# Performance work log

Measured on AMD Instinct MI355X. Metric: run time of the kernel, lower is better.

Reference implementation:

```python
import jax, jax.numpy as jnp
import numpy as np

L = 64      # number of physical sites (hilbert.size)
d = 2       # local Hilbert dimension (hilbert.local_size)
D = 8       # bond dimension
CHI = 4     # Kraus dimension
B = 1024    # batch of configurations


def setup_inputs() -> dict:
    key = jax.random.key(0)
    k1, k2 = jax.random.split(key)
    # local quantum-number indices, rows and columns concatenated: [B, 2L]
    qn = jax.random.randint(k1, (B, 2 * L), 0, d, dtype=jnp.int32)
    # MPDO unit-cell tensors: small random perturbation added to identity in the (D, D) slots
    iden = jnp.broadcast_to(jnp.eye(D, dtype=jnp.float32)[None, None, :, :, None], (L, d, D, D, CHI))
    tensors = 0.01 * jax.random.normal(k2, (L, d, D, D, CHI), dtype=jnp.float32) + iden
    return {"qn": qn, "tensors": tensors}


def reference(qn, tensors):
    D2 = D * D
    qn_r = qn[:, :L].T  # [L, B]
    qn_c = qn[:, L:].T  # [L, B]
    edge0 = jnp.broadcast_to(jnp.eye(D2, dtype=tensors.dtype), (qn.shape[0], D2, D2))

    def step(edge, site):
        T, ir, ic = site                 # T: [d, D, D, CHI], ir/ic: [B]
        Tr = T[ir]                       # [B, D, D, CHI]
        Tc = jnp.conj(T[ic])             # [B, D, D, CHI]
        m = jnp.einsum('bijk,blmk->biljm', Tr, Tc).reshape(-1, D2, D2)
        return jnp.matmul(edge, m), None

    step = jax.checkpoint(step)
    edge, _ = jax.lax.scan(step, edge0, (tensors, qn_r, qn_c))
    rho = jnp.trace(edge, axis1=-2, axis2=-1)   # [B]
    return jnp.log(rho.astype(jnp.complex64))
```

## Files before the change

kernel.cpp:

```cpp
#include <hip/hip_runtime.h>
#include <math.h>


#define NSITES 64
#define NPAIRS 32

typedef float f32x16 __attribute__((ext_vector_type(16)));
typedef int   i32x8  __attribute__((ext_vector_type(8)));

union AFrag { uint4 q[2]; i32x8 v; };

#define PACK4(P, A0, A1, A2, A3)                                               \
    asm("v_cvt_pk_fp8_f32 %0, %1, %2" : "=v"(P) : "v"(A0), "v"(A1));           \
    asm("v_cvt_pk_fp8_f32 %0, %1, %2 op_sel:[0,0,1]" : "+v"(P) : "v"(A2), "v"(A3));

#define MFMA64(A, B, C)                                                        \
    __builtin_amdgcn_mfma_scale_f32_32x32x64_f8f6f4(                           \
        (A), (B), (C), 0, 0, 0, 0x7F7F7F7F, 0, 0x7F7F7F7F)

__global__ __launch_bounds__(64)
void mpdo_prep2f8k(const float* __restrict__ T, uint4* __restrict__ Mf8) {
    const int blk = blockIdx.x;
    const int pair = blk >> 4, combo = blk & 15;
    const int c0 = combo >> 2, c1 = combo & 3;
    const int ir0 = c0 >> 1, ic0 = c0 & 1, ir1 = c1 >> 1, ic1 = c1 & 1;
    const int lane = threadIdx.x;
    const int site0 = 2 * pair, site1 = 2 * pair + 1;

    __shared__ float sT0[256], sT1[256], sT2[256], sT3[256];
    __shared__ float sPA[16 * 64], sPB[16 * 64];

    *(float4*)&sT0[lane * 4] = *(const float4*)(T + ((size_t)(site0 * 2 + ir0)) * 256 + lane * 4);
    *(float4*)&sT1[lane * 4] = *(const float4*)(T + ((size_t)(site0 * 2 + ic0)) * 256 + lane * 4);
    *(float4*)&sT2[lane * 4] = *(const float4*)(T + ((size_t)(site1 * 2 + ir1)) * 256 + lane * 4);
    *(float4*)&sT3[lane * 4] = *(const float4*)(T + ((size_t)(site1 * 2 + ic1)) * 256 + lane * 4);
    __syncthreads();

    {
        const int i = lane >> 3, j = lane & 7;
        float pa[4][4], pb[4][4];
#pragma unroll
        for (int k = 0; k < 4; ++k)
#pragma unroll
            for (int jp = 0; jp < 4; ++jp) { pa[k][jp] = 0.0f; pb[k][jp] = 0.0f; }
#pragma unroll
        for (int a = 0; a < 8; ++a) {
            float4 x0 = *(const float4*)&sT0[(i * 8 + a) * 4];
            float4 y0 = *(const float4*)&sT2[(a * 8 + j) * 4];
            float4 x1 = *(const float4*)&sT1[(i * 8 + a) * 4];
            float4 y1 = *(const float4*)&sT3[(a * 8 + j) * 4];
            const float xk0[4] = {x0.x, x0.y, x0.z, x0.w};
            const float yj0[4] = {y0.x, y0.y, y0.z, y0.w};
            const float xk1[4] = {x1.x, x1.y, x1.z, x1.w};
            const float yj1[4] = {y1.x, y1.y, y1.z, y1.w};
#pragma unroll
            for (int k = 0; k < 4; ++k)
#pragma unroll
                for (int jp = 0; jp < 4; ++jp) {
                    pa[k][jp] = fmaf(xk0[k], yj0[jp], pa[k][jp]);
                    pb[k][jp] = fmaf(xk1[k], yj1[jp], pb[k][jp]);
                }
        }
#pragma unroll
        for (int k = 0; k < 4; ++k)
#pragma unroll
            for (int jp = 0; jp < 4; ++jp) {
                sPA[(k * 4 + jp) * 64 + lane] = pa[k][jp];
                sPB[(k * 4 + jp) * 64 + lane] = pb[k][jp];
            }
    }
    __syncthreads();

    const int h = lane >> 5, r = lane & 31, m = r & 7, j2 = r >> 3;
    float acc2[2][32];
#pragma unroll
    for (int ti = 0; ti < 2; ++ti)
#pragma unroll
        for (int e = 0; e < 32; ++e) acc2[ti][e] = 0.0f;

#pragma unroll 4
    for (int c = 0; c < 16; ++c) {
        float pav[2][4], pbv[8];
#pragma unroll
        for (int ti = 0; ti < 2; ++ti)
#pragma unroll
            for (int ii = 0; ii < 4; ++ii)
                pav[ti][ii] = sPA[c * 64 + (4 * h + ii) * 8 + (4 * ti + j2)];
#pragma unroll
        for (int l = 0; l < 8; ++l) pbv[l] = sPB[c * 64 + l * 8 + m];
#pragma unroll
        for (int ti = 0; ti < 2; ++ti)
#pragma unroll
            for (int ii = 0; ii < 4; ++ii)
#pragma unroll
                for (int l = 0; l < 8; ++l)
                    acc2[ti][8 * ii + l] = fmaf(pav[ti][ii], pbv[l], acc2[ti][8 * ii + l]);
    }

#pragma unroll
    for (int ti = 0; ti < 2; ++ti) {
        unsigned dw[8];
#pragma unroll
        for (int j = 0; j < 8; ++j) {
            float v[4];
#pragma unroll
            for (int s = 0; s < 4; ++s) {
                float wv = acc2[ti][4 * j + s] * 0.0625f;
                if (ti == h && (4 * j + s) == r) wv -= 1.0f;
                v[s] = wv;
            }
            PACK4(dw[j], v[0], v[1], v[2], v[3])
        }
        Mf8[((size_t)(pair * 16 + combo) * 4 + ti * 2 + 0) * 64 + lane] =
            make_uint4(dw[0], dw[1], dw[2], dw[3]);
        Mf8[((size_t)(pair * 16 + combo) * 4 + ti * 2 + 1) * 64 + lane] =
            make_uint4(dw[4], dw[5], dw[6], dw[7]);
    }
}

__global__ __launch_bounds__(64, 1)
void mpdo_mfmaK(const int* __restrict__ qn, const uint4* __restrict__ Mf8,
                float* __restrict__ out) {
    const int b = blockIdx.x;
    const int lane = threadIdx.x;
    const int* qb = qn + (size_t)b * (2 * NSITES);
    const int pi = lane & 31;
    const int pc = (qb[2 * pi] << 3) | (qb[64 + 2 * pi] << 2) |
                   (qb[2 * pi + 1] << 1) | (qb[64 + 2 * pi + 1]);
    const unsigned long long m3 = __ballot(pc & 8);
    const unsigned long long m2 = __ballot(pc & 4);
    const unsigned long long m1 = __ballot(pc & 2);
    const unsigned long long m0 = __ballot(pc & 1);
    const int col = lane & 31, hh = lane >> 5;
    const int laneoff = lane * 16;

    f32x16 acc[2][2];
#pragma unroll
    for (int rt = 0; rt < 2; ++rt)
#pragma unroll
        for (int ct = 0; ct < 2; ++ct)
#pragma unroll
            for (int g = 0; g < 16; ++g) {
                int row = (g & 3) + 8 * (g >> 2) + 4 * hh;
                acc[rt][ct][g] = (rt == ct && row == col) ? 1.0f : 0.0f;
            }

    const char* Mbase = (const char*)Mf8;
    AFrag A0[2], A1[2], A2[2];

#define COMBO(T_) ((int)(((((m3) >> (T_)) & 1ull) << 3) | ((((m2) >> (T_)) & 1ull) << 2) | \
                         ((((m1) >> (T_)) & 1ull) << 1) | (((m0) >> (T_)) & 1ull)))
#define LOADF(DST, PIDX)                                                       \
    {                                                                          \
        int c_ = COMBO(PIDX);                                                  \
        const char* nb_ = Mbase + (((size_t)(PIDX) * 16 + c_) << 12) + laneoff;\
        DST[0].q[0] = *(const uint4*)(nb_ + 0 * 1024);                         \
        DST[0].q[1] = *(const uint4*)(nb_ + 1 * 1024);                         \
        DST[1].q[0] = *(const uint4*)(nb_ + 2 * 1024);                         \
        DST[1].q[1] = *(const uint4*)(nb_ + 3 * 1024);                         \
    }

#define MAKE_BCOL(BV, CT)                                                      \
    {                                                                          \
        _Pragma("unroll")                                                      \
        for (int q = 0; q < 4; ++q) {                                          \
            unsigned p0, p1;                                                   \
            PACK4(p0, acc[0][CT][4 * q + 0], acc[0][CT][4 * q + 1],            \
                      acc[0][CT][4 * q + 2], acc[0][CT][4 * q + 3])            \
            PACK4(p1, acc[1][CT][4 * q + 0], acc[1][CT][4 * q + 1],            \
                      acc[1][CT][4 * q + 2], acc[1][CT][4 * q + 3])            \
            asm("v_permlane32_swap_b32 %0, %1" : "+v"(p0), "+v"(p1));          \
            BV[2 * q] = (int)p0; BV[2 * q + 1] = (int)p1;                      \
        }                                                                      \
    }

#define SITE_BODY(T_, CUR, NXT)                                                \
    {                                                                          \
        if ((T_) + 2 < 32) { LOADF(NXT, (T_) + 2) }                            \
        i32x8 b0, b1;                                                          \
        MAKE_BCOL(b0, 0)                                                       \
        MAKE_BCOL(b1, 1)                                                       \
        acc[0][0] = MFMA64(CUR[0].v, b0, acc[0][0]);                           \
        acc[0][1] = MFMA64(CUR[0].v, b1, acc[0][1]);                           \
        acc[1][0] = MFMA64(CUR[1].v, b0, acc[1][0]);                           \
        acc[1][1] = MFMA64(CUR[1].v, b1, acc[1][1]);                           \
    }

    LOADF(A0, 0)
    LOADF(A1, 1)

    SITE_BODY(0,  A0, A2) SITE_BODY(1,  A1, A0) SITE_BODY(2,  A2, A1)
    SITE_BODY(3,  A0, A2) SITE_BODY(4,  A1, A0) SITE_BODY(5,  A2, A1)
    SITE_BODY(6,  A0, A2) SITE_BODY(7,  A1, A0) SITE_BODY(8,  A2, A1)
    SITE_BODY(9,  A0, A2) SITE_BODY(10, A1, A0) SITE_BODY(11, A2, A1)
    SITE_BODY(12, A0, A2) SITE_BODY(13, A1, A0) SITE_BODY(14, A2, A1)
    SITE_BODY(15, A0, A2) SITE_BODY(16, A1, A0) SITE_BODY(17, A2, A1)
    SITE_BODY(18, A0, A2) SITE_BODY(19, A1, A0) SITE_BODY(20, A2, A1)
    SITE_BODY(21, A0, A2) SITE_BODY(22, A1, A0) SITE_BODY(23, A2, A1)
    SITE_BODY(24, A0, A2) SITE_BODY(25, A1, A0) SITE_BODY(26, A2, A1)
    SITE_BODY(27, A0, A2) SITE_BODY(28, A1, A0) SITE_BODY(29, A2, A1)
    SITE_BODY(30, A0, A2) SITE_BODY(31, A1, A0)
#undef SITE_BODY
#undef MAKE_BCOL
#undef LOADF
#undef COMBO

    float diag = 0.0f;
#pragma unroll
    for (int tt = 0; tt < 2; ++tt)
#pragma unroll
        for (int g = 0; g < 16; ++g) {
            int row = (g & 3) + 8 * (g >> 2) + 4 * hh;
            if (row == col) diag += acc[tt][tt][g];
        }
#pragma unroll
    for (int off = 32; off >= 1; off >>= 1)
        diag += __shfl_xor(diag, off, 64);

    if (lane == 0) {
        float tr = diag;
        float re = logf(fabsf(tr)) + 64.0f * 1.3862943611198906f;
        float im = (tr < 0.0f) ? 3.14159265358979323846f : 0.0f;
        out[2 * b]     = re;
        out[2 * b + 1] = im;
    }
}

#define DD 8
#define KCHI 4
__global__ __launch_bounds__(64, 1)
void mpdo_chain(const int* __restrict__ qn, const float* __restrict__ T,
                float* __restrict__ out) {
    const int b = blockIdx.x;
    const int lane = threadIdx.x;
    __shared__ float sA[KCHI][DD][DD];
    __shared__ float sB[KCHI][DD][DD];
    float E[DD][DD];
#pragma unroll
    for (int i = 0; i < DD; ++i)
#pragma unroll
        for (int l = 0; l < DD; ++l) E[i][l] = (i * DD + l == lane) ? 1.0f : 0.0f;
    const int* qb = qn + (size_t)b * (2 * NSITES);
    int ir0 = qb[0], ic0 = qb[NSITES];
    float4 aP = *reinterpret_cast<const float4*>(T + (size_t)ir0 * 256 + lane * 4);
    float4 bP = *reinterpret_cast<const float4*>(T + (size_t)ic0 * 256 + lane * 4);
    const int li = lane >> 3, lj = lane & 7;
#pragma unroll 1
    for (int site = 0; site < NSITES; ++site) {
        __syncthreads();
        sA[0][li][lj] = 0.5f * aP.x; sA[1][li][lj] = 0.5f * aP.y;
        sA[2][li][lj] = 0.5f * aP.z; sA[3][li][lj] = 0.5f * aP.w;
        sB[0][li][lj] = 0.5f * bP.x; sB[1][li][lj] = 0.5f * bP.y;
        sB[2][li][lj] = 0.5f * bP.z; sB[3][li][lj] = 0.5f * bP.w;
        __syncthreads();
        if (site + 1 < NSITES) {
            int irn = qb[site + 1], icn = qb[NSITES + site + 1];
            aP = *reinterpret_cast<const float4*>(T + ((size_t)(site + 1) * 2 + irn) * 256 + lane * 4);
            bP = *reinterpret_cast<const float4*>(T + ((size_t)(site + 1) * 2 + icn) * 256 + lane * 4);
        }
        float Ep[DD][DD];
#pragma unroll
        for (int j = 0; j < DD; ++j)
#pragma unroll
            for (int m = 0; m < DD; ++m) Ep[j][m] = 0.0f;
#pragma unroll 1
        for (int k = 0; k < KCHI; ++k) {
            float tmp[DD][DD];
#pragma unroll
            for (int l = 0; l < DD; ++l) {
                const float4* bp = reinterpret_cast<const float4*>(&sB[k][l][0]);
                float4 b0 = bp[0], b1 = bp[1];
                float brow[DD] = {b0.x, b0.y, b0.z, b0.w, b1.x, b1.y, b1.z, b1.w};
                if (l == 0) {
#pragma unroll
                    for (int i = 0; i < DD; ++i)
#pragma unroll
                        for (int m = 0; m < DD; ++m) tmp[i][m] = E[i][0] * brow[m];
                } else {
#pragma unroll
                    for (int i = 0; i < DD; ++i)
#pragma unroll
                        for (int m = 0; m < DD; ++m)
                            tmp[i][m] = fmaf(E[i][l], brow[m], tmp[i][m]);
                }
            }
#pragma unroll
            for (int i = 0; i < DD; ++i) {
                const float4* ap = reinterpret_cast<const float4*>(&sA[k][i][0]);
                float4 a0 = ap[0], a1 = ap[1];
                float arow[DD] = {a0.x, a0.y, a0.z, a0.w, a1.x, a1.y, a1.z, a1.w};
#pragma unroll
                for (int j = 0; j < DD; ++j)
#pragma unroll
                    for (int m = 0; m < DD; ++m)
                        Ep[j][m] = fmaf(arow[j], tmp[i][m], Ep[j][m]);
            }
        }
#pragma unroll
        for (int i = 0; i < DD; ++i)
#pragma unroll
            for (int l = 0; l < DD; ++l) E[i][l] = Ep[i][l];
    }
    float diag = 0.0f;
#pragma unroll
    for (int i = 0; i < DD; ++i)
#pragma unroll
        for (int l = 0; l < DD; ++l) diag += (i * DD + l == lane) ? E[i][l] : 0.0f;
#pragma unroll
    for (int off = 32; off >= 1; off >>= 1) diag += __shfl_xor(diag, off, 64);
    if (lane == 0) {
        float tr = diag;
        out[2 * b]     = logf(fabsf(tr)) + 64.0f * 1.3862943611198906f;
        out[2 * b + 1] = (tr < 0.0f) ? 3.14159265358979323846f : 0.0f;
    }
}

extern "C" void kernel_launch(void* const* d_in, const int* in_sizes, int n_in,
                              void* d_out, int out_size, void* d_ws, size_t ws_size,
                              hipStream_t stream) {
    const int*   qn  = (const int*)d_in[0];
    const float* T   = (const float*)d_in[1];
    float*       out = (float*)d_out;
    const int B = in_sizes[0] / (2 * NSITES);
    const size_t WS_F8 = (size_t)NPAIRS * 16 * 4 * 64 * 16;
    if (ws_size >= WS_F8) {
        uint4* Mf8 = (uint4*)d_ws;
        mpdo_prep2f8k<<<dim3(NPAIRS * 16), dim3(64), 0, stream>>>(T, Mf8);
        mpdo_mfmaK<<<dim3(B), dim3(64), 0, stream>>>(qn, Mf8, out);
    } else {
        mpdo_chain<<<dim3(B), dim3(64), 0, stream>>>(qn, T, out);
    }
}
```

Before: 26.00 us.

## Split site chain into two independent halves interleaved for MFMA latency hiding

The 32-step serial chain of 64x64 FP8 MFMA products is split into two independent 16-step chains (pairs 0-15 and 16-31), interleaved so each half's MFMAs can hide the other's dependency latency. The final trace is computed as trace(L0*L1) via a transposed dot product, with the second half's matrix staged through padded shared memory. This doubles accumulator and prefetch register usage and adds an LDS round-trip and barrier at the end.

```diff
diff --git a/kernel.cpp b/kernel.cpp
--- a/kernel.cpp
+++ b/kernel.cpp
@@ -119,10 +119,11 @@
 }
 
 __global__ __launch_bounds__(64, 1)
-void mpdo_mfmaK(const int* __restrict__ qn, const uint4* __restrict__ Mf8,
-                float* __restrict__ out) {
+void mpdo_mfmaK2(const int* __restrict__ qn, const uint4* __restrict__ Mf8,
+                 float* __restrict__ out) {
     const int b = blockIdx.x;
     const int lane = threadIdx.x;
+    __shared__ float sL[64 * 65];
     const int* qb = qn + (size_t)b * (2 * NSITES);
     const int pi = lane & 31;
     const int pc = (qb[2 * pi] << 3) | (qb[64 + 2 * pi] << 2) |
@@ -134,7 +135,7 @@
     const int col = lane & 31, hh = lane >> 5;
     const int laneoff = lane * 16;
 
-    f32x16 acc[2][2];
+    f32x16 acc0[2][2], acc1[2][2];
 #pragma unroll
     for (int rt = 0; rt < 2; ++rt)
 #pragma unroll
@@ -142,11 +143,14 @@
 #pragma unroll
             for (int g = 0; g < 16; ++g) {
                 int row = (g & 3) + 8 * (g >> 2) + 4 * hh;
-                acc[rt][ct][g] = (rt == ct && row == col) ? 1.0f : 0.0f;
+                float v = (rt == ct && row == col) ? 1.0f : 0.0f;
+                acc0[rt][ct][g] = v;
+                acc1[rt][ct][g] = v;
             }
 
     const char* Mbase = (const char*)Mf8;
     AFrag A0[2], A1[2], A2[2];
+    AFrag C0[2], C1[2], C2[2];
 
 #define COMBO(T_) ((int)(((((m3) >> (T_)) & 1ull) << 3) | ((((m2) >> (T_)) & 1ull) << 2) | \
                          ((((m1) >> (T_)) & 1ull) << 1) | (((m0) >> (T_)) & 1ull)))
@@ -160,69 +164,84 @@
         DST[1].q[1] = *(const uint4*)(nb_ + 3 * 1024);                         \
     }
 
-#define MAKE_BCOL(BV, CT)                                                      \
+#define MAKE_BCOL(BV, ACC, CT)                                                 \
     {                                                                          \
         _Pragma("unroll")                                                      \
         for (int q = 0; q < 4; ++q) {                                          \
             unsigned p0, p1;                                                   \
-            PACK4(p0, acc[0][CT][4 * q + 0], acc[0][CT][4 * q + 1],            \
-                      acc[0][CT][4 * q + 2], acc[0][CT][4 * q + 3])            \
-            PACK4(p1, acc[1][CT][4 * q + 0], acc[1][CT][4 * q + 1],            \
-                      acc[1][CT][4 * q + 2], acc[1][CT][4 * q + 3])            \
+            PACK4(p0, ACC[0][CT][4 * q + 0], ACC[0][CT][4 * q + 1],            \
+                      ACC[0][CT][4 * q + 2], ACC[0][CT][4 * q + 3])            \
+            PACK4(p1, ACC[1][CT][4 * q + 0], ACC[1][CT][4 * q + 1],            \
+                      ACC[1][CT][4 * q + 2], ACC[1][CT][4 * q + 3])            \
             asm("v_permlane32_swap_b32 %0, %1" : "+v"(p0), "+v"(p1));          \
             BV[2 * q] = (int)p0; BV[2 * q + 1] = (int)p1;                      \
         }                                                                      \
     }
 
-#define SITE_BODY(T_, CUR, NXT)                                                \
+#define STEP1(T_, LIM_, ACC, CUR, NXT)                                         \
     {                                                                          \
-        if ((T_) + 2 < 32) { LOADF(NXT, (T_) + 2) }                            \
+        if ((T_) + 2 < (LIM_)) { LOADF(NXT, (T_) + 2) }                        \
         i32x8 b0, b1;                                                          \
-        MAKE_BCOL(b0, 0)                                                       \
-        MAKE_BCOL(b1, 1)                                                       \
-        acc[0][0] = MFMA64(CUR[0].v, b0, acc[0][0]);                           \
-        acc[0][1] = MFMA64(CUR[0].v, b1, acc[0][1]);                           \
-        acc[1][0] = MFMA64(CUR[1].v, b0, acc[1][0]);                           \
-        acc[1][1] = MFMA64(CUR[1].v, b1, acc[1][1]);                           \
-    }
-
-    LOADF(A0, 0)
-    LOADF(A1, 1)
-
-    SITE_BODY(0,  A0, A2) SITE_BODY(1,  A1, A0) SITE_BODY(2,  A2, A1)
-    SITE_BODY(3,  A0, A2) SITE_BODY(4,  A1, A0) SITE_BODY(5,  A2, A1)
-    SITE_BODY(6,  A0, A2) SITE_BODY(7,  A1, A0) SITE_BODY(8,  A2, A1)
-    SITE_BODY(9,  A0, A2) SITE_BODY(10, A1, A0) SITE_BODY(11, A2, A1)
-    SITE_BODY(12, A0, A2) SITE_BODY(13, A1, A0) SITE_BODY(14, A2, A1)
-    SITE_BODY(15, A0, A2) SITE_BODY(16, A1, A0) SITE_BODY(17, A2, A1)
-    SITE_BODY(18, A0, A2) SITE_BODY(19, A1, A0) SITE_BODY(20, A2, A1)
-    SITE_BODY(21, A0, A2) SITE_BODY(22, A1, A0) SITE_BODY(23, A2, A1)
-    SITE_BODY(24, A0, A2) SITE_BODY(25, A1, A0) SITE_BODY(26, A2, A1)
-    SITE_BODY(27, A0, A2) SITE_BODY(28, A1, A0) SITE_BODY(29, A2, A1)
-    SITE_BODY(30, A0, A2) SITE_BODY(31, A1, A0)
-#undef SITE_BODY
+        MAKE_BCOL(b0, ACC, 0)                                                  \
+        MAKE_BCOL(b1, ACC, 1)                                                  \
+        ACC[0][0] = MFMA64(CUR[0].v, b0, ACC[0][0]);                           \
+        ACC[0][1] = MFMA64(CUR[0].v, b1, ACC[0][1]);                           \
+        ACC[1][0] = MFMA64(CUR[1].v, b0, ACC[1][0]);                           \
+        ACC[1][1] = MFMA64(CUR[1].v, b1, ACC[1][1]);                           \
+    }
+
+#define DSTEP(I_, X, XN, Y, YN)                                                \
+    STEP1((I_),      16, acc0, X, XN)                                          \
+    STEP1(16 + (I_), 32, acc1, Y, YN)
+
+    LOADF(A0, 0)  LOADF(A1, 1)
+    LOADF(C0, 16) LOADF(C1, 17)
+
+    DSTEP(0,  A0, A2, C0, C2) DSTEP(1,  A1, A0, C1, C0) DSTEP(2,  A2, A1, C2, C1)
+    DSTEP(3,  A0, A2, C0, C2) DSTEP(4,  A1, A0, C1, C0) DSTEP(5,  A2, A1, C2, C1)
+    DSTEP(6,  A0, A2, C0, C2) DSTEP(7,  A1, A0, C1, C0) DSTEP(8,  A2, A1, C2, C1)
+    DSTEP(9,  A0, A2, C0, C2) DSTEP(10, A1, A0, C1, C0) DSTEP(11, A2, A1, C2, C1)
+    DSTEP(12, A0, A2, C0, C2) DSTEP(13, A1, A0, C1, C0) DSTEP(14, A2, A1, C2, C1)
+    DSTEP(15, A0, A2, C0, C2)
+#undef DSTEP
+#undef STEP1
 #undef MAKE_BCOL
 #undef LOADF
 #undef COMBO
 
-    float diag = 0.0f;
-#pragma unroll
-    for (int tt = 0; tt < 2; ++tt)
-#pragma unroll
-        for (int g = 0; g < 16; ++g) {
-            int row = (g & 3) + 8 * (g >> 2) + 4 * hh;
-            if (row == col) diag += acc[tt][tt][g];
-        }
-#pragma unroll
-    for (int off = 32; off >= 1; off >>= 1)
-        diag += __shfl_xor(diag, off, 64);
-
-    if (lane == 0) {
-        float tr = diag;
-        float re = logf(fabsf(tr)) + 64.0f * 1.3862943611198906f;
-        float im = (tr < 0.0f) ? 3.14159265358979323846f : 0.0f;
-        out[2 * b]     = re;
-        out[2 * b + 1] = im;
+#pragma unroll
+    for (int rt = 0; rt < 2; ++rt)
+#pragma unroll
+        for (int ct = 0; ct < 2; ++ct)
+#pragma unroll
+            for (int g = 0; g < 16; ++g) {
+                int p = 32 * rt + (g & 3) + 8 * (g >> 2) + 4 * hh;
+                int q = 32 * ct + col;
+                sL[p * 65 + q] = acc1[rt][ct][g];
+            }
+    __syncthreads();
+    {
+        float dot = 0.0f;
+#pragma unroll
+        for (int rt = 0; rt < 2; ++rt)
+#pragma unroll
+            for (int ct = 0; ct < 2; ++ct)
+#pragma unroll
+                for (int g = 0; g < 16; ++g) {
+                    int p = 32 * rt + (g & 3) + 8 * (g >> 2) + 4 * hh;
+                    int q = 32 * ct + col;
+                    dot = fmaf(acc0[rt][ct][g], sL[q * 65 + p], dot);
+                }
+#pragma unroll
+        for (int off = 32; off >= 1; off >>= 1)
+            dot += __shfl_xor(dot, off, 64);
+        if (lane == 0) {
+            float tr = dot;
+            float re = logf(fabsf(tr)) + 64.0f * 1.3862943611198906f;
+            float im = (tr < 0.0f) ? 3.14159265358979323846f : 0.0f;
+            out[2 * b]     = re;
+            out[2 * b + 1] = im;
+        }
     }
 }
 
@@ -326,7 +345,7 @@
     if (ws_size >= WS_F8) {
         uint4* Mf8 = (uint4*)d_ws;
         mpdo_prep2f8k<<<dim3(NPAIRS * 16), dim3(64), 0, stream>>>(T, Mf8);
-        mpdo_mfmaK<<<dim3(B), dim3(64), 0, stream>>>(qn, Mf8, out);
+        mpdo_mfmaK2<<<dim3(B), dim3(64), 0, stream>>>(qn, Mf8, out);
     } else {
         mpdo_chain<<<dim3(B), dim3(64), 0, stream>>>(qn, T, out);
     }
```

Measured after the change: 25.79 us. Within noise of the previous version (-0.8%).

## Split site-pair chain across two waves and combine via trace of product

Applied to the files above, without the earlier changes.

Each batch element now uses two wavefronts, each multiplying 16 of the 32 pair matrices in sequence, which halves the serial MFMA dependency chain. The two partial products go through shared memory, and the trace of their product is computed as an elementwise dot of one with the transpose of the other. This adds a shared-memory exchange, a barrier and more per-block LDS, and it doubles the wave count per block.

```diff
diff --git a/kernel.cpp b/kernel.cpp
--- a/kernel.cpp
+++ b/kernel.cpp
@@ -118,11 +118,13 @@
     }
 }
 
-__global__ __launch_bounds__(64, 1)
-void mpdo_mfmaK(const int* __restrict__ qn, const uint4* __restrict__ Mf8,
-                float* __restrict__ out) {
+__global__ __launch_bounds__(128)
+void mpdo_mfmaW2(const int* __restrict__ qn, const uint4* __restrict__ Mf8,
+                 float* __restrict__ out) {
     const int b = blockIdx.x;
-    const int lane = threadIdx.x;
+    const int w = threadIdx.x >> 6;
+    const int lane = threadIdx.x & 63;
+    __shared__ float sL[2][64 * 65];
     const int* qb = qn + (size_t)b * (2 * NSITES);
     const int pi = lane & 31;
     const int pc = (qb[2 * pi] << 3) | (qb[64 + 2 * pi] << 2) |
@@ -133,6 +135,7 @@
     const unsigned long long m0 = __ballot(pc & 1);
     const int col = lane & 31, hh = lane >> 5;
     const int laneoff = lane * 16;
+    const int s0 = 16 * w;
 
     f32x16 acc[2][2];
 #pragma unroll
@@ -152,8 +155,9 @@
                          ((((m1) >> (T_)) & 1ull) << 1) | (((m0) >> (T_)) & 1ull)))
 #define LOADF(DST, PIDX)                                                       \
     {                                                                          \
-        int c_ = COMBO(PIDX);                                                  \
-        const char* nb_ = Mbase + (((size_t)(PIDX) * 16 + c_) << 12) + laneoff;\
+        int p_ = (PIDX);                                                       \
+        int c_ = COMBO(p_);                                                    \
+        const char* nb_ = Mbase + (((size_t)p_ * 16 + c_) << 12) + laneoff;    \
         DST[0].q[0] = *(const uint4*)(nb_ + 0 * 1024);                         \
         DST[0].q[1] = *(const uint4*)(nb_ + 1 * 1024);                         \
         DST[1].q[0] = *(const uint4*)(nb_ + 2 * 1024);                         \
@@ -174,9 +178,9 @@
         }                                                                      \
     }
 
-#define SITE_BODY(T_, CUR, NXT)                                                \
+#define SITE_BODY(I_, CUR, NXT)                                                \
     {                                                                          \
-        if ((T_) + 2 < 32) { LOADF(NXT, (T_) + 2) }                            \
+        if ((I_) + 2 < 16) { LOADF(NXT, s0 + (I_) + 2) }                       \
         i32x8 b0, b1;                                                          \
         MAKE_BCOL(b0, 0)                                                       \
         MAKE_BCOL(b1, 1)                                                       \
@@ -186,43 +190,53 @@
         acc[1][1] = MFMA64(CUR[1].v, b1, acc[1][1]);                           \
     }
 
-    LOADF(A0, 0)
-    LOADF(A1, 1)
+    LOADF(A0, s0)
+    LOADF(A1, s0 + 1)
 
     SITE_BODY(0,  A0, A2) SITE_BODY(1,  A1, A0) SITE_BODY(2,  A2, A1)
     SITE_BODY(3,  A0, A2) SITE_BODY(4,  A1, A0) SITE_BODY(5,  A2, A1)
     SITE_BODY(6,  A0, A2) SITE_BODY(7,  A1, A0) SITE_BODY(8,  A2, A1)
     SITE_BODY(9,  A0, A2) SITE_BODY(10, A1, A0) SITE_BODY(11, A2, A1)
     SITE_BODY(12, A0, A2) SITE_BODY(13, A1, A0) SITE_BODY(14, A2, A1)
-    SITE_BODY(15, A0, A2) SITE_BODY(16, A1, A0) SITE_BODY(17, A2, A1)
-    SITE_BODY(18, A0, A2) SITE_BODY(19, A1, A0) SITE_BODY(20, A2, A1)
-    SITE_BODY(21, A0, A2) SITE_BODY(22, A1, A0) SITE_BODY(23, A2, A1)
-    SITE_BODY(24, A0, A2) SITE_BODY(25, A1, A0) SITE_BODY(26, A2, A1)
-    SITE_BODY(27, A0, A2) SITE_BODY(28, A1, A0) SITE_BODY(29, A2, A1)
-    SITE_BODY(30, A0, A2) SITE_BODY(31, A1, A0)
+    SITE_BODY(15, A0, A2)
 #undef SITE_BODY
 #undef MAKE_BCOL
 #undef LOADF
 #undef COMBO
 
-    float diag = 0.0f;
-#pragma unroll
-    for (int tt = 0; tt < 2; ++tt)
-#pragma unroll
-        for (int g = 0; g < 16; ++g) {
-            int row = (g & 3) + 8 * (g >> 2) + 4 * hh;
-            if (row == col) diag += acc[tt][tt][g];
-        }
-#pragma unroll
-    for (int off = 32; off >= 1; off >>= 1)
-        diag += __shfl_xor(diag, off, 64);
-
-    if (lane == 0) {
-        float tr = diag;
-        float re = logf(fabsf(tr)) + 64.0f * 1.3862943611198906f;
-        float im = (tr < 0.0f) ? 3.14159265358979323846f : 0.0f;
-        out[2 * b]     = re;
-        out[2 * b + 1] = im;
+#pragma unroll
+    for (int rt = 0; rt < 2; ++rt)
+#pragma unroll
+        for (int ct = 0; ct < 2; ++ct)
+#pragma unroll
+            for (int g = 0; g < 16; ++g) {
+                int p = 32 * rt + (g & 3) + 8 * (g >> 2) + 4 * hh;
+                int q = 32 * ct + col;
+                sL[w][p * 65 + q] = acc[rt][ct][g];
+            }
+    __syncthreads();
+    if (w == 0) {
+        float dot = 0.0f;
+#pragma unroll
+        for (int rt = 0; rt < 2; ++rt)
+#pragma unroll
+            for (int ct = 0; ct < 2; ++ct)
+#pragma unroll
+                for (int g = 0; g < 16; ++g) {
+                    int p = 32 * rt + (g & 3) + 8 * (g >> 2) + 4 * hh;
+                    int q = 32 * ct + col;
+                    dot = fmaf(acc[rt][ct][g], sL[1][q * 65 + p], dot);
+                }
+#pragma unroll
+        for (int off = 32; off >= 1; off >>= 1)
+            dot += __shfl_xor(dot, off, 64);
+        if (lane == 0) {
+            float tr = dot;
+            float re = logf(fabsf(tr)) + 64.0f * 1.3862943611198906f;
+            float im = (tr < 0.0f) ? 3.14159265358979323846f : 0.0f;
+            out[2 * b]     = re;
+            out[2 * b + 1] = im;
+        }
     }
 }
 
@@ -326,7 +340,7 @@
     if (ws_size >= WS_F8) {
         uint4* Mf8 = (uint4*)d_ws;
         mpdo_prep2f8k<<<dim3(NPAIRS * 16), dim3(64), 0, stream>>>(T, Mf8);
-        mpdo_mfmaK<<<dim3(B), dim3(64), 0, stream>>>(qn, Mf8, out);
+        mpdo_mfmaW2<<<dim3(B), dim3(128), 0, stream>>>(qn, Mf8, out);
     } else {
         mpdo_chain<<<dim3(B), dim3(64), 0, stream>>>(qn, T, out);
     }
```

Measured after the change: 25.50 us (median of 2 runs). No clear change (-1.9%).
